# Kernel optimization log

Hardware: AMD Instinct MI355X
Metric: run time of the kernel (lower is better)

Reference implementation:

```python
import jax, jax.numpy as jnp
import numpy as np

M, K, N = 8192, 4096, 4096
SCALE_D = 0.05  # per-tensor activation quant step

def setup_inputs() -> dict:
    key = jax.random.key(0)
    k1, k2, k3, k4 = jax.random.split(key, 4)
    x = jax.random.normal(k1, (M, K), jnp.float32)
    # already-quantized int8 weight, stored transposed as in the module: [K, N]
    q_weight = jax.random.randint(k2, (K, N), -127, 128).astype(jnp.int8)
    # per-tensor activation quant: act_scale = 1/scale_d, act_offset = 0
    act_scale = jnp.asarray(1.0 / SCALE_D, jnp.float32)
    act_offset = jnp.asarray(0.0, jnp.float32)
    # per-output-channel weight scales -> deq_scale = scale_d * scale_w, shape [N]
    scale_w = jax.random.uniform(k3, (N,), jnp.float32, 0.001, 0.01)
    deq_scale = (SCALE_D * scale_w).astype(jnp.float32)
    # int32 bias = round(bias_f / (scale_d * scale_w))
    bias_f = jax.random.normal(k4, (N,), jnp.float32) * 0.1
    bias_i32 = jnp.round(bias_f / deq_scale).astype(jnp.int32)
    return {"x": x, "q_weight": q_weight, "act_scale": act_scale,
            "act_offset": act_offset, "deq_scale": deq_scale, "bias_i32": bias_i32}

def reference(x, q_weight, act_scale, act_offset, deq_scale, bias_i32):
    # npu_quantize(div_mode=False): q = clamp(round(x * scale + offset), int8)
    qx = jnp.clip(jnp.round(x * act_scale + act_offset), -128.0, 127.0).astype(jnp.int8)
    # npu_quant_matmul: int8 GEMM accumulated in int32, + int32 bias, * deq_scale
    acc = jnp.matmul(qx.astype(jnp.int32), q_weight.astype(jnp.int32),
                     preferred_element_type=jnp.int32)  # [M, N] int32
    out = (acc + bias_i32[None, :]).astype(jnp.float32) * deq_scale[None, :]
    return out
```

## Files before the change

kernel.cpp:

```cpp
#include <hip/hip_runtime.h>
#include <stdint.h>

#define GM 8192
#define GK 4096
#define GN 4096

typedef int v4i __attribute__((ext_vector_type(4)));

__device__ __forceinline__ void async_load16(const void* gptr, void* lptr) {
  __builtin_amdgcn_global_load_lds(
      (const __attribute__((address_space(1))) void*)gptr,
      (__attribute__((address_space(3))) void*)lptr,
      16 , 0 , 0 );
}

#define TBLK ((GN / 64) * (GK / 64))
#define QBLK (GM * GK / 4 / 256)

__global__ __launch_bounds__(256) void prep_kernel(
    const float* __restrict__ x, int8_t* __restrict__ qx,
    const float* __restrict__ scale_p, const float* __restrict__ off_p,
    const int* __restrict__ B, int8_t* __restrict__ Bt) {
  __shared__ int tile32[64][65];
  const int b = blockIdx.x;
  const int t = threadIdx.x;
  if (b < TBLK) {
    const int n0 = (b & 63) * 64;
    const int k0 = (b >> 6) * 64;
#pragma unroll
    for (int r = 0; r < 4; ++r) {
      const int kl = r * 16 + (t >> 4);
      const int nl = (t & 15) * 4;
      const int4 v = *(const int4*)(B + (size_t)(k0 + kl) * GN + n0 + nl);
      *(int4*)&tile32[kl][nl] = v;
    }
    __syncthreads();
    const int nl = t >> 2;
    const int kc = (t & 3) * 16;
    v4i out;
#pragma unroll
    for (int w = 0; w < 4; ++w) {
      int p = 0;
#pragma unroll
      for (int j = 0; j < 4; ++j)
        p |= (tile32[kc + w * 4 + j][nl] & 0xff) << (8 * j);
      out[w] = p;
    }
    *(v4i*)(Bt + (size_t)(n0 + nl) * GK + k0 + kc) = out;
  } else {
    const int i = (b - TBLK) * 256 + t;
    const float s = scale_p[0], o = off_p[0];
    const float4 f = ((const float4*)x)[i];
    float a0 = fminf(fmaxf(rintf(f.x * s + o), -128.f), 127.f);
    float b0 = fminf(fmaxf(rintf(f.y * s + o), -128.f), 127.f);
    float c0 = fminf(fmaxf(rintf(f.z * s + o), -128.f), 127.f);
    float d0 = fminf(fmaxf(rintf(f.w * s + o), -128.f), 127.f);
    int packed = (((int)a0) & 0xff) | ((((int)b0) & 0xff) << 8) |
                 ((((int)c0) & 0xff) << 16) | ((((int)d0) & 0xff) << 24);
    ((int*)qx)[i] = packed;
  }
}

__global__ __launch_bounds__(256) void gemm_i8_kernel(
    const int8_t* __restrict__ A, const int8_t* __restrict__ Bt,
    const int* __restrict__ bias, const float* __restrict__ deq,
    float* __restrict__ C) {
  __shared__ __align__(16) int8_t Alds[2][128 * 64];
  __shared__ __align__(16) int8_t Blds[2][128 * 64];

  const int t = threadIdx.x;
  const int lane = t & 63;
  const int wave = t >> 6;
  const int m0 = blockIdx.y * 128;
  const int n0 = blockIdx.x * 128;
  const int wm = (wave >> 1) * 64;
  const int wn = (wave & 1) * 64;

  v4i acc[4][4];
  const v4i vzero = {0, 0, 0, 0};
#pragma unroll
  for (int mi = 0; mi < 4; ++mi)
#pragma unroll
    for (int ni = 0; ni < 4; ++ni) acc[mi][ni] = vzero;

  const int srow = t >> 2;
  const int scol = (t & 3) * 16;
  const int8_t* ag = A + (size_t)(m0 + srow) * GK + scol;
  const int8_t* bg = Bt + (size_t)(n0 + srow) * GK + scol;
  const size_t rg = (size_t)64 * GK;
  int8_t* al = &Alds[0][0] + t * 16;
  int8_t* bl = &Blds[0][0] + t * 16;

  const int fr = lane & 15;
  const int kg = (lane >> 4) * 16;

  for (int k0 = 0; k0 < GK; k0 += 128) {
    __syncthreads();
    async_load16(ag + k0, al);
    async_load16(ag + rg + k0, al + 4096);
    async_load16(bg + k0, bl);
    async_load16(bg + rg + k0, bl + 4096);
    async_load16(ag + k0 + 64, al + 8192);
    async_load16(ag + rg + k0 + 64, al + 12288);
    async_load16(bg + k0 + 64, bl + 8192);
    async_load16(bg + rg + k0 + 64, bl + 12288);
    __syncthreads();

#pragma unroll
    for (int s = 0; s < 2; ++s) {
      v4i af[4], bf[4];
#pragma unroll
      for (int i = 0; i < 4; ++i) {
        af[i] = *(const v4i*)(&Alds[s][0] + (size_t)(wm + i * 16 + fr) * 64 + kg);
        bf[i] = *(const v4i*)(&Blds[s][0] + (size_t)(wn + i * 16 + fr) * 64 + kg);
      }
#pragma unroll
      for (int mi = 0; mi < 4; ++mi)
#pragma unroll
        for (int ni = 0; ni < 4; ++ni)
          acc[mi][ni] =
              __builtin_amdgcn_mfma_i32_16x16x64_i8(af[mi], bf[ni], acc[mi][ni], 0, 0, 0);
    }
  }

  const int col = lane & 15;
  const int rq = (lane >> 4) * 4;
#pragma unroll
  for (int ni = 0; ni < 4; ++ni) {
    const int gc = n0 + wn + ni * 16 + col;
    const float d = deq[gc];
    const int bs = bias[gc];
#pragma unroll
    for (int mi = 0; mi < 4; ++mi) {
      const int gr = m0 + wm + mi * 16 + rq;
#pragma unroll
      for (int r = 0; r < 4; ++r)
        C[(size_t)(gr + r) * GN + gc] = (float)(acc[mi][ni][r] + bs) * d;
    }
  }
}

extern "C" void kernel_launch(void* const* d_in, const int* in_sizes, int n_in,
                              void* d_out, int out_size, void* d_ws, size_t ws_size,
                              hipStream_t stream) {
  const float* x = (const float*)d_in[0];
  const int* qw = (const int*)d_in[1];
  const float* act_scale = (const float*)d_in[2];
  const float* act_offset = (const float*)d_in[3];
  const float* deq = (const float*)d_in[4];
  const int* bias = (const int*)d_in[5];
  float* out = (float*)d_out;

  int8_t* qx = (int8_t*)d_ws;
  int8_t* Bt = (int8_t*)d_ws + (size_t)GM * GK;

  prep_kernel<<<TBLK + QBLK, 256, 0, stream>>>(x, qx, act_scale, act_offset, qw, Bt);
  gemm_i8_kernel<<<dim3(GN / 128, GM / 128), 256, 0, stream>>>(qx, Bt, bias, deq, out);
}
```

Baseline: 410.1 us.

## Rewrite int8 GEMM with 256x256 tiles, pipelined async loads and swizzled LDS

The GEMM moves from 128x128 tiles with 4 waves to 256x256 tiles with 8 waves. Global-to-LDS async loads are split into quarter-tile stages that run ahead across double-buffered 128-wide K slices, with MFMA quads interleaved between barriers and s_setprio raised around the compute. LDS rows get an XOR swizzle to avoid bank conflicts, and the block index is remapped for L2 locality. This targets load stalls and barrier bubbles in the old loop, at the cost of 128KB of LDS per block, higher register pressure, and hand-placed waitcnt logic that is easy to get wrong.

```diff
diff --git a/kernel.cpp b/kernel.cpp
--- a/kernel.cpp
+++ b/kernel.cpp
@@ -61,83 +61,203 @@
   }
 }
 
-__global__ __launch_bounds__(256) void gemm_i8_kernel(
+#define NT (GK / 128)
+
+__global__ __launch_bounds__(512, 2) void gemm_i8_kernel(
     const int8_t* __restrict__ A, const int8_t* __restrict__ Bt,
     const int* __restrict__ bias, const float* __restrict__ deq,
     float* __restrict__ C) {
-  __shared__ __align__(16) int8_t Alds[2][128 * 64];
-  __shared__ __align__(16) int8_t Blds[2][128 * 64];
+  __shared__ __align__(16) int8_t Al[2][2][128 * 128];
+  __shared__ __align__(16) int8_t Bl[2][2][128 * 128];
 
   const int t = threadIdx.x;
   const int lane = t & 63;
-  const int wave = t >> 6;
-  const int m0 = blockIdx.y * 128;
-  const int n0 = blockIdx.x * 128;
-  const int wm = (wave >> 1) * 64;
-  const int wn = (wave & 1) * 64;
-
-  v4i acc[4][4];
-  const v4i vzero = {0, 0, 0, 0};
-#pragma unroll
-  for (int mi = 0; mi < 4; ++mi)
-#pragma unroll
-    for (int ni = 0; ni < 4; ++ni) acc[mi][ni] = vzero;
-
-  const int srow = t >> 2;
-  const int scol = (t & 3) * 16;
-  const int8_t* ag = A + (size_t)(m0 + srow) * GK + scol;
-  const int8_t* bg = Bt + (size_t)(n0 + srow) * GK + scol;
-  const size_t rg = (size_t)64 * GK;
-  int8_t* al = &Alds[0][0] + t * 16;
-  int8_t* bl = &Blds[0][0] + t * 16;
+  const int wid = t >> 6;
+
+  const int bid = blockIdx.x;
+  const int swz = (bid & 7) * 64 + (bid >> 3);
+  const int m0 = (swz >> 4) * 256;
+  const int n0 = (swz & 15) * 256;
+
+  const int ahalf = wid >> 2;
+  const int bhalf = (wid & 3) >> 1;
+  const int bloc = (wid & 1) * 64;
+  const int wm = ahalf * 128;
+  const int wn = (wid & 3) * 64;
 
   const int fr = lane & 15;
-  const int kg = (lane >> 4) * 16;
-
-  for (int k0 = 0; k0 < GK; k0 += 128) {
-    __syncthreads();
-    async_load16(ag + k0, al);
-    async_load16(ag + rg + k0, al + 4096);
-    async_load16(bg + k0, bl);
-    async_load16(bg + rg + k0, bl + 4096);
-    async_load16(ag + k0 + 64, al + 8192);
-    async_load16(ag + rg + k0 + 64, al + 12288);
-    async_load16(bg + k0 + 64, bl + 8192);
-    async_load16(bg + rg + k0 + 64, bl + 12288);
-    __syncthreads();
-
-#pragma unroll
-    for (int s = 0; s < 2; ++s) {
-      v4i af[4], bf[4];
-#pragma unroll
-      for (int i = 0; i < 4; ++i) {
-        af[i] = *(const v4i*)(&Alds[s][0] + (size_t)(wm + i * 16 + fr) * 64 + kg);
-        bf[i] = *(const v4i*)(&Blds[s][0] + (size_t)(wn + i * 16 + fr) * 64 + kg);
-      }
-#pragma unroll
-      for (int mi = 0; mi < 4; ++mi)
-#pragma unroll
-        for (int ni = 0; ni < 4; ++ni)
-          acc[mi][ni] =
-              __builtin_amdgcn_mfma_i32_16x16x64_i8(af[mi], bf[ni], acc[mi][ni], 0, 0, 0);
-    }
+  const int kq = lane >> 4;
+  const int sw0 = ((kq) ^ (fr & 7)) * 16;
+  const int sw1 = ((4 + kq) ^ (fr & 7)) * 16;
+
+  const int srow = t >> 3;
+  const int lg16 = (((t & 7) ^ (srow & 7)) * 16);
+  const int ldst = t * 16;
+
+  v4i acc[8][4];
+  const v4i vz = {0, 0, 0, 0};
+#pragma unroll
+  for (int m = 0; m < 8; ++m)
+#pragma unroll
+    for (int n = 0; n < 4; ++n) acc[m][n] = vz;
+
+#define STAGE(hh)                                                         \
+  do {                                                                    \
+    const int h_ = (hh);                                                  \
+    const int T_ = h_ >> 2, c_ = h_ & 3, b_ = T_ & 1;                     \
+    const size_t ko_ = (size_t)T_ * 128 + lg16;                           \
+    if (c_ < 2) {                                                         \
+      const int8_t* s_ = A + (size_t)(m0 + c_ * 128 + srow) * GK + ko_;   \
+      int8_t* d_ = &Al[b_][c_][0] + ldst;                                 \
+      async_load16(s_, d_);                                               \
+      async_load16(s_ + (size_t)64 * GK, d_ + 8192);                      \
+    } else {                                                              \
+      const int8_t* s_ =                                                  \
+          Bt + (size_t)(n0 + (c_ - 2) * 128 + srow) * GK + ko_;           \
+      int8_t* d_ = &Bl[b_][c_ - 2][0] + ldst;                             \
+      async_load16(s_, d_);                                               \
+      async_load16(s_ + (size_t)64 * GK, d_ + 8192);                      \
+    }                                                                     \
+  } while (0)
+
+#define READ_A(dst, swz_)                                                 \
+  do {                                                                    \
+    const int8_t* p_ = &Al[buf][ahalf][0] + fr * 128 + (swz_);            \
+    _Pragma("unroll") for (int i_ = 0; i_ < 8; ++i_)                      \
+        dst[i_] = *(const v4i*)(p_ + i_ * 2048);                          \
+  } while (0)
+
+#define READ_B(dst, swz_)                                                 \
+  do {                                                                    \
+    const int8_t* p_ = &Bl[buf][bhalf][0] + (bloc + fr) * 128 + (swz_);   \
+    _Pragma("unroll") for (int i_ = 0; i_ < 4; ++i_)                      \
+        dst[i_] = *(const v4i*)(p_ + i_ * 2048);                          \
+  } while (0)
+
+#define QUAD(AF, BF, MB)                                                  \
+  do {                                                                    \
+    _Pragma("unroll") for (int mi_ = 0; mi_ < 4; ++mi_) {                 \
+      _Pragma("unroll") for (int ni_ = 0; ni_ < 4; ++ni_) {               \
+        acc[(MB) + mi_][ni_] = __builtin_amdgcn_mfma_i32_16x16x64_i8(     \
+            AF[(MB) + mi_], BF[ni_], acc[(MB) + mi_][ni_], 0, 0, 0);      \
+      }                                                                   \
+    }                                                                     \
+  } while (0)
+
+#define LGKM0 asm volatile("s_waitcnt lgkmcnt(0)" ::: "memory")
+#define VMC4 asm volatile("s_waitcnt vmcnt(4)" ::: "memory")
+#define VMC0 asm volatile("s_waitcnt vmcnt(0)" ::: "memory")
+#define BAR __builtin_amdgcn_s_barrier()
+
+  v4i a0[8], a1[8], b0[4], b1[4];
+
+  STAGE(0); STAGE(1); STAGE(2); STAGE(3); STAGE(4); STAGE(5);
+  VMC4;
+  BAR;
+
+#pragma unroll 2
+  for (int kt = 0; kt < NT - 2; ++kt) {
+    const int buf = kt & 1;
+    const int hb = 4 * kt + 6;
+    READ_A(a0, sw0);
+    READ_B(b0, sw0);
+    STAGE(hb);
+    BAR;
+    LGKM0;
+    __builtin_amdgcn_s_setprio(1);
+    QUAD(a0, b0, 0);
+    __builtin_amdgcn_s_setprio(0);
+    BAR;
+    READ_A(a1, sw1);
+    STAGE(hb + 1);
+    BAR;
+    LGKM0;
+    __builtin_amdgcn_s_setprio(1);
+    QUAD(a0, b0, 4);
+    __builtin_amdgcn_s_setprio(0);
+    BAR;
+    READ_B(b1, sw1);
+    STAGE(hb + 2);
+    BAR;
+    LGKM0;
+    __builtin_amdgcn_s_setprio(1);
+    QUAD(a1, b1, 0);
+    __builtin_amdgcn_s_setprio(0);
+    BAR;
+    STAGE(hb + 3);
+    __builtin_amdgcn_s_setprio(1);
+    QUAD(a1, b1, 4);
+    __builtin_amdgcn_s_setprio(0);
+    VMC4;
+    BAR;
+  }
+  {
+    const int buf = 0;
+    READ_A(a0, sw0);
+    READ_B(b0, sw0);
+    STAGE(126);
+    BAR;
+    LGKM0;
+    __builtin_amdgcn_s_setprio(1);
+    QUAD(a0, b0, 0);
+    __builtin_amdgcn_s_setprio(0);
+    BAR;
+    READ_A(a1, sw1);
+    STAGE(127);
+    BAR;
+    LGKM0;
+    __builtin_amdgcn_s_setprio(1);
+    QUAD(a0, b0, 4);
+    __builtin_amdgcn_s_setprio(0);
+    BAR;
+    READ_B(b1, sw1);
+    BAR;
+    LGKM0;
+    __builtin_amdgcn_s_setprio(1);
+    QUAD(a1, b1, 0);
+    __builtin_amdgcn_s_setprio(0);
+    BAR;
+    __builtin_amdgcn_s_setprio(1);
+    QUAD(a1, b1, 4);
+    __builtin_amdgcn_s_setprio(0);
+    VMC0;
+    BAR;
+  }
+  {
+    const int buf = 1;
+    READ_A(a0, sw0);
+    READ_B(b0, sw0);
+    READ_A(a1, sw1);
+    READ_B(b1, sw1);
+    QUAD(a0, b0, 0);
+    QUAD(a0, b0, 4);
+    QUAD(a1, b1, 0);
+    QUAD(a1, b1, 4);
   }
 
   const int col = lane & 15;
   const int rq = (lane >> 4) * 4;
 #pragma unroll
-  for (int ni = 0; ni < 4; ++ni) {
-    const int gc = n0 + wn + ni * 16 + col;
+  for (int n = 0; n < 4; ++n) {
+    const int gc = n0 + wn + n * 16 + col;
     const float d = deq[gc];
     const int bs = bias[gc];
 #pragma unroll
-    for (int mi = 0; mi < 4; ++mi) {
-      const int gr = m0 + wm + mi * 16 + rq;
+    for (int m = 0; m < 8; ++m) {
+      const int gr = m0 + wm + m * 16 + rq;
 #pragma unroll
       for (int r = 0; r < 4; ++r)
-        C[(size_t)(gr + r) * GN + gc] = (float)(acc[mi][ni][r] + bs) * d;
+        C[(size_t)(gr + r) * GN + gc] = (float)(acc[m][n][r] + bs) * d;
     }
   }
+#undef STAGE
+#undef READ_A
+#undef READ_B
+#undef QUAD
+#undef LGKM0
+#undef VMC4
+#undef VMC0
+#undef BAR
 }
 
 extern "C" void kernel_launch(void* const* d_in, const int* in_sizes, int n_in,
@@ -155,5 +275,5 @@
   int8_t* Bt = (int8_t*)d_ws + (size_t)GM * GK;
 
   prep_kernel<<<TBLK + QBLK, 256, 0, stream>>>(x, qx, act_scale, act_offset, qw, Bt);
-  gemm_i8_kernel<<<dim3(GN / 128, GM / 128), 256, 0, stream>>>(qx, Bt, bias, deq, out);
-}
+  gemm_i8_kernel<<<dim3((GM / 256) * (GN / 256)), 512, 0, stream>>>(qx, Bt, bias, deq, out);
+}
```

Result: faster. 397.6 us (-3.1%).

## Rewrite int8 GEMM with 256x256 tiles, double-buffered LDS and swizzled prefetch

Applied to the files above, without the earlier changes.

The GEMM moves to 256x256 output tiles using 512 threads and a 1D grid with a block swizzle for L2 locality. LDS is double-buffered so the next K tile loads asynchronously while MFMAs run on the current one, with register double-buffering of fragments. An XOR swizzle on LDS addresses avoids bank conflicts, and s_setprio raises priority around the MFMA bursts. It uses 128KB of LDS and more accumulator registers per thread, which may limit occupancy.

```diff
diff --git a/kernel.cpp b/kernel.cpp
--- a/kernel.cpp
+++ b/kernel.cpp
@@ -61,83 +61,142 @@
   }
 }
 
-__global__ __launch_bounds__(256) void gemm_i8_kernel(
+#define NT (GK / 128)
+
+__global__ __launch_bounds__(512, 2) void gemm_i8_kernel(
     const int8_t* __restrict__ A, const int8_t* __restrict__ Bt,
     const int* __restrict__ bias, const float* __restrict__ deq,
     float* __restrict__ C) {
-  __shared__ __align__(16) int8_t Alds[2][128 * 64];
-  __shared__ __align__(16) int8_t Blds[2][128 * 64];
+  __shared__ __align__(16) int8_t Al[2][2][128 * 128];
+  __shared__ __align__(16) int8_t Bl[2][2][128 * 128];
 
   const int t = threadIdx.x;
   const int lane = t & 63;
-  const int wave = t >> 6;
-  const int m0 = blockIdx.y * 128;
-  const int n0 = blockIdx.x * 128;
-  const int wm = (wave >> 1) * 64;
-  const int wn = (wave & 1) * 64;
-
-  v4i acc[4][4];
-  const v4i vzero = {0, 0, 0, 0};
-#pragma unroll
-  for (int mi = 0; mi < 4; ++mi)
-#pragma unroll
-    for (int ni = 0; ni < 4; ++ni) acc[mi][ni] = vzero;
-
-  const int srow = t >> 2;
-  const int scol = (t & 3) * 16;
-  const int8_t* ag = A + (size_t)(m0 + srow) * GK + scol;
-  const int8_t* bg = Bt + (size_t)(n0 + srow) * GK + scol;
-  const size_t rg = (size_t)64 * GK;
-  int8_t* al = &Alds[0][0] + t * 16;
-  int8_t* bl = &Blds[0][0] + t * 16;
+  const int wid = t >> 6;
+
+  const int bid = blockIdx.x;
+  const int swz = (bid & 7) * 64 + (bid >> 3);
+  const int m0 = (swz >> 4) * 256;
+  const int n0 = (swz & 15) * 256;
+
+  const int ahalf = wid >> 2;
+  const int bhalf = (wid & 3) >> 1;
+  const int bloc = (wid & 1) * 64;
+  const int wm = ahalf * 128;
+  const int wn = (wid & 3) * 64;
 
   const int fr = lane & 15;
-  const int kg = (lane >> 4) * 16;
-
-  for (int k0 = 0; k0 < GK; k0 += 128) {
-    __syncthreads();
-    async_load16(ag + k0, al);
-    async_load16(ag + rg + k0, al + 4096);
-    async_load16(bg + k0, bl);
-    async_load16(bg + rg + k0, bl + 4096);
-    async_load16(ag + k0 + 64, al + 8192);
-    async_load16(ag + rg + k0 + 64, al + 12288);
-    async_load16(bg + k0 + 64, bl + 8192);
-    async_load16(bg + rg + k0 + 64, bl + 12288);
-    __syncthreads();
-
-#pragma unroll
-    for (int s = 0; s < 2; ++s) {
-      v4i af[4], bf[4];
-#pragma unroll
-      for (int i = 0; i < 4; ++i) {
-        af[i] = *(const v4i*)(&Alds[s][0] + (size_t)(wm + i * 16 + fr) * 64 + kg);
-        bf[i] = *(const v4i*)(&Blds[s][0] + (size_t)(wn + i * 16 + fr) * 64 + kg);
-      }
-#pragma unroll
-      for (int mi = 0; mi < 4; ++mi)
-#pragma unroll
-        for (int ni = 0; ni < 4; ++ni)
-          acc[mi][ni] =
-              __builtin_amdgcn_mfma_i32_16x16x64_i8(af[mi], bf[ni], acc[mi][ni], 0, 0, 0);
-    }
+  const int kq = lane >> 4;
+  const int sw0 = ((kq) ^ (fr & 7)) * 16;
+  const int sw1 = ((4 + kq) ^ (fr & 7)) * 16;
+
+  const int srow = t >> 3;
+  const int lg16 = (((t & 7) ^ (srow & 7)) * 16);
+  const int ldst = t * 16;
+
+  v4i acc[8][4];
+  const v4i vz = {0, 0, 0, 0};
+#pragma unroll
+  for (int m = 0; m < 8; ++m)
+#pragma unroll
+    for (int n = 0; n < 4; ++n) acc[m][n] = vz;
+
+#define STAGE_TILE(T)                                                  \
+  do {                                                                 \
+    const int T_ = (T), b_ = T_ & 1;                                   \
+    const size_t ko_ = (size_t)T_ * 128 + lg16;                        \
+    const int8_t* sa_ = A + (size_t)(m0 + srow) * GK + ko_;            \
+    int8_t* da_ = &Al[b_][0][0] + ldst;                                \
+    async_load16(sa_, da_);                                            \
+    async_load16(sa_ + (size_t)64 * GK, da_ + 8192);                   \
+    async_load16(sa_ + (size_t)128 * GK, da_ + 16384);                 \
+    async_load16(sa_ + (size_t)192 * GK, da_ + 24576);                 \
+    const int8_t* sb_ = Bt + (size_t)(n0 + srow) * GK + ko_;           \
+    int8_t* db_ = &Bl[b_][0][0] + ldst;                                \
+    async_load16(sb_, db_);                                            \
+    async_load16(sb_ + (size_t)64 * GK, db_ + 8192);                   \
+    async_load16(sb_ + (size_t)128 * GK, db_ + 16384);                 \
+    async_load16(sb_ + (size_t)192 * GK, db_ + 24576);                 \
+  } while (0)
+
+#define READ_A(dst, bb, swz_)                                          \
+  do {                                                                 \
+    const int8_t* p_ = &Al[bb][ahalf][0] + fr * 128 + (swz_);          \
+    _Pragma("unroll") for (int i_ = 0; i_ < 8; ++i_)                   \
+        dst[i_] = *(const v4i*)(p_ + i_ * 2048);                       \
+  } while (0)
+
+#define READ_B(dst, bb, swz_)                                          \
+  do {                                                                 \
+    const int8_t* p_ = &Bl[bb][bhalf][0] + (bloc + fr) * 128 + (swz_); \
+    _Pragma("unroll") for (int i_ = 0; i_ < 4; ++i_)                   \
+        dst[i_] = *(const v4i*)(p_ + i_ * 2048);                       \
+  } while (0)
+
+#define QUAD(AF, BF, MB)                                               \
+  do {                                                                 \
+    _Pragma("unroll") for (int mi_ = 0; mi_ < 4; ++mi_) {              \
+      _Pragma("unroll") for (int ni_ = 0; ni_ < 4; ++ni_) {            \
+        acc[(MB) + mi_][ni_] = __builtin_amdgcn_mfma_i32_16x16x64_i8(  \
+            AF[(MB) + mi_], BF[ni_], acc[(MB) + mi_][ni_], 0, 0, 0);   \
+      }                                                                \
+    }                                                                  \
+  } while (0)
+
+  v4i a0[8], b0[4], a1[8], b1[4];
+
+  STAGE_TILE(0);
+  asm volatile("s_waitcnt vmcnt(0)\ns_barrier" ::: "memory");
+  READ_A(a0, 0, sw0);
+  READ_B(b0, 0, sw0);
+
+#pragma unroll 2
+  for (int kt = 0; kt < NT - 1; ++kt) {
+    const int buf = kt & 1;
+    READ_A(a1, buf, sw1);
+    READ_B(b1, buf, sw1);
+    STAGE_TILE(kt + 1);
+    __builtin_amdgcn_s_setprio(1);
+    QUAD(a0, b0, 0);
+    QUAD(a0, b0, 4);
+    __builtin_amdgcn_s_setprio(0);
+    asm volatile("s_waitcnt lgkmcnt(0) vmcnt(0)\n\ts_barrier" ::: "memory");
+    READ_A(a0, buf ^ 1, sw0);
+    READ_B(b0, buf ^ 1, sw0);
+    __builtin_amdgcn_s_setprio(1);
+    QUAD(a1, b1, 0);
+    QUAD(a1, b1, 4);
+    __builtin_amdgcn_s_setprio(0);
+  }
+  {
+    const int buf = (NT - 1) & 1;
+    READ_A(a1, buf, sw1);
+    READ_B(b1, buf, sw1);
+    QUAD(a0, b0, 0);
+    QUAD(a0, b0, 4);
+    QUAD(a1, b1, 0);
+    QUAD(a1, b1, 4);
   }
 
   const int col = lane & 15;
   const int rq = (lane >> 4) * 4;
 #pragma unroll
-  for (int ni = 0; ni < 4; ++ni) {
-    const int gc = n0 + wn + ni * 16 + col;
+  for (int n = 0; n < 4; ++n) {
+    const int gc = n0 + wn + n * 16 + col;
     const float d = deq[gc];
     const int bs = bias[gc];
 #pragma unroll
-    for (int mi = 0; mi < 4; ++mi) {
-      const int gr = m0 + wm + mi * 16 + rq;
+    for (int m = 0; m < 8; ++m) {
+      const int gr = m0 + wm + m * 16 + rq;
 #pragma unroll
       for (int r = 0; r < 4; ++r)
-        C[(size_t)(gr + r) * GN + gc] = (float)(acc[mi][ni][r] + bs) * d;
+        C[(size_t)(gr + r) * GN + gc] = (float)(acc[m][n][r] + bs) * d;
     }
   }
+#undef STAGE_TILE
+#undef READ_A
+#undef READ_B
+#undef QUAD
 }
 
 extern "C" void kernel_launch(void* const* d_in, const int* in_sizes, int n_in,
@@ -155,5 +214,5 @@
   int8_t* Bt = (int8_t*)d_ws + (size_t)GM * GK;
 
   prep_kernel<<<TBLK + QBLK, 256, 0, stream>>>(x, qx, act_scale, act_offset, qw, Bt);
-  gemm_i8_kernel<<<dim3(GN / 128, GM / 128), 256, 0, stream>>>(qx, Bt, bias, deq, out);
-}
+  gemm_i8_kernel<<<dim3((GM / 256) * (GN / 256)), 512, 0, stream>>>(qx, Bt, bias, deq, out);
+}
```

New measurement: 390.6 us. -4.8%, faster.
